# Kernel optimization log

Measured on AMD Instinct MI355X. Metric: run time of the kernel, lower is better.

Reference implementation:

```python
import jax, jax.numpy as jnp
import numpy as np

N, E, DIN, GB, GD, LB, LD, G = 50000, 640000, 64, 128, 4, 256, 2, 1024


def setup_inputs() -> dict:
    key = jax.random.key(0)
    ks = jax.random.split(key, 20)
    p = lambda k, shape: (jax.random.normal(k, shape, dtype=jnp.float32) * 0.05)
    return {
        "x": jax.random.normal(ks[0], (N, DIN), dtype=jnp.float32),
        "edge_index": jax.random.randint(ks[1], (2, E), 0, N, dtype=jnp.int64),
        "batch": jnp.sort(jax.random.randint(ks[2], (N,), 0, G, dtype=jnp.int64)),
        "num_graphs": G,
        "W0": p(ks[3], (DIN, GB)), "b0": p(ks[4], (GB,)),
        "Wg": p(ks[5], (GD, GB, GB)), "bg": p(ks[6], (GD, GB)),
        "gamma_g": jnp.ones((GD, GB), jnp.float32), "beta_g": jnp.zeros((GD, GB), jnp.float32),
        "Wl0": p(ks[7], (GB, LB)), "bl0": p(ks[8], (LB,)),
        "Wl": p(ks[9], (LD, LB, LB)), "bl": p(ks[10], (LD, LB)),
        "gamma_l": jnp.ones((LD, LB), jnp.float32), "beta_l": jnp.zeros((LD, LB), jnp.float32),
        "Wout": p(ks[11], (LB, 2)), "bout": p(ks[12], (2,)),
    }


def reference(x, edge_index, batch, num_graphs, W0, b0, Wg, bg, gamma_g, beta_g,
              Wl0, bl0, Wl, bl, gamma_l, beta_l, Wout, bout):
    n = x.shape[0]
    src, dst = edge_index[0], edge_index[1]
    # GCN degree normalization with self loops: deg = 1 + in-degree
    deg = jax.ops.segment_sum(jnp.ones(src.shape[0], x.dtype), dst, num_segments=n) + 1.0
    dinv = jax.lax.rsqrt(deg)                 # deg^{-1/2}
    enorm = dinv[src] * dinv[dst]             # [E] edge norm
    snorm = dinv * dinv                       # [N] self-loop norm (deg^{-1})

    def gcn(h, W, b):
        hw = h @ W                                            # [N, GB]
        agg = jax.ops.segment_sum(hw[src] * enorm[:, None], dst, num_segments=n)
        return agg + hw * snorm[:, None] + b

    def bn(h, g, bt):  # training-mode batchnorm (biased var), eps=1e-5
        m = h.mean(0)
        v = h.var(0)
        return (h - m) * jax.lax.rsqrt(v + 1e-5) * g + bt

    h = jax.nn.relu(gcn(x, W0, b0))
    for i in range(Wg.shape[0]):
        h = jax.nn.relu(bn(gcn(h, Wg[i], bg[i]), gamma_g[i], beta_g[i]))
    # global_add_pool
    hp = jax.ops.segment_sum(h, batch, num_segments=num_graphs)  # [G, GB]
    h = jax.nn.relu(hp @ Wl0 + bl0)
    for i in range(Wl.shape[0]):
        h = jax.nn.relu(bn(h @ Wl[i] + bl[i], gamma_l[i], beta_l[i]))
    return h @ Wout + bout
```

## Files before the change

kernel.cpp:

```cpp
#include <hip/hip_runtime.h>

#define NN 50000
#define EE 640000
#define DINv 64
#define GBv 128
#define GDv 4
#define LBv 256
#define LDv 2
#define GGv 1024

#define NB 196
#define BCAP 4096
#define BTILE 4096
#define NBT ((EE + BTILE - 1) / BTILE)

#define NTILES ((NN + 63) / 64)
#define UPN (NN * 16)
#define CONVN (DINv * GBv + GDv * GBv * GBv)
#define ZEXT 320

typedef _Float16 f16x8 __attribute__((ext_vector_type(8)));
typedef float f32x4 __attribute__((ext_vector_type(4)));

__device__ __forceinline__ float h2f(ushort u) {
  union { ushort u; _Float16 h; } x;
  x.u = u;
  return (float)x.h;
}
__device__ __forceinline__ ushort f2h(float f) {
  union { ushort u; _Float16 h; } x;
  x.h = (_Float16)f;
  return x.u;
}


__global__ __launch_bounds__(256) void k_bucket(const int* __restrict__ ei,
                                                int* __restrict__ bcnt,
                                                uint* __restrict__ bkt) {
  __shared__ int lcnt[NB];
  __shared__ int lbase[NB];
  __shared__ int gbase[NB];
  __shared__ int ls[256];
  __shared__ uint stage[BTILE];
  __shared__ ushort sb[BTILE];
  int tid = threadIdx.x;
  int t0 = blockIdx.x * BTILE;
  int cnt = min(BTILE, EE - t0);
  for (int i = tid; i < NB; i += 256) lcnt[i] = 0;
  __syncthreads();

  uint en[16];
  int bb[16], rk[16];
  int nper = (cnt + 255) >> 8;
  for (int k = 0; k < nper; k++) {
    int e = k * 256 + tid;
    if (e < cnt) {
      int src = ei[t0 + e];
      int dst = ei[EE + t0 + e];
      int b = dst >> 8;
      en[k] = ((uint)src << 8) | (uint)(dst & 255);
      bb[k] = b;
      rk[k] = atomicAdd(&lcnt[b], 1);
    } else {
      bb[k] = -1;
    }
  }
  __syncthreads();

  int v = (tid < NB) ? lcnt[tid] : 0;
  ls[tid] = v;
  __syncthreads();
  for (int off = 1; off < 256; off <<= 1) {
    int t = (tid >= off) ? ls[tid - off] : 0;
    __syncthreads();
    ls[tid] += t;
    __syncthreads();
  }
  if (tid < NB) {
    lbase[tid] = ls[tid] - v;
    gbase[tid] = atomicAdd(&bcnt[tid], v);
  }
  __syncthreads();

  for (int k = 0; k < nper; k++) {
    if (bb[k] >= 0) {
      int slot = lbase[bb[k]] + rk[k];
      stage[slot] = en[k];
      sb[slot] = (ushort)bb[k];
    }
  }
  __syncthreads();

  for (int i = tid; i < cnt; i += 256) {
    int b = sb[i];
    bkt[(size_t)b * BCAP + gbase[b] + (i - lbase[b])] = stage[i];
  }
}


__global__ __launch_bounds__(256) void k_csr(const uint* __restrict__ bkt,
                                             const int* __restrict__ bcnt,
                                             int* __restrict__ offs,
                                             float* __restrict__ dinv,
                                             int* __restrict__ col,
                                             int* __restrict__ deg,
                                             int* __restrict__ ghist) {
  __shared__ int lhist[256];
  __shared__ int lofs[256];
  __shared__ int lcur[256];
  __shared__ int lsb[256];
  __shared__ int lh2[64];
  int b = blockIdx.x;
  int tid = threadIdx.x;
  int bv = (tid < NB) ? bcnt[tid] : 0;
  lsb[tid] = bv;
  lhist[tid] = 0;
  if (tid < 64) lh2[tid] = 0;
  __syncthreads();
  for (int off = 1; off < 256; off <<= 1) {
    int t = (tid >= off) ? lsb[tid - off] : 0;
    __syncthreads();
    lsb[tid] += t;
    __syncthreads();
  }
  int cnt = bcnt[b];
  int rawbase = lsb[b] - cnt;
  int pbase = ((rawbase + 7) & ~7) + b * 4096;
  const uint* B = bkt + (size_t)b * BCAP;
  for (int i = tid; i < cnt; i += 256) atomicAdd(&lhist[B[i] & 255], 1);
  __syncthreads();
  int v = lhist[tid];
  int pv = (v + 15) & ~15;
  lofs[tid] = pv;
  __syncthreads();
  for (int off = 1; off < 256; off <<= 1) {
    int t = (tid >= off) ? lofs[tid - off] : 0;
    __syncthreads();
    lofs[tid] += t;
    __syncthreads();
  }
  int excl = lofs[tid] - pv;
  int n = b * 256 + tid;
  if (n < NN) {
    offs[n] = pbase + excl;
    dinv[n] = rsqrtf((float)(v + 1));
    deg[n] = v;
    atomicAdd(&lh2[min(v, 63)], 1);
    for (int k = v; k < pv; k++) col[pbase + excl + k] = NN;
  }
  lcur[tid] = excl;
  __syncthreads();
  if (tid < 64 && lh2[tid]) atomicAdd(&ghist[tid], lh2[tid]);
  if (b == 0 && tid == 0) dinv[NN] = 0.f;
  for (int i = tid; i < cnt; i += 256) {
    uint e = B[i];
    int p = atomicAdd(&lcur[e & 255], 1);
    col[pbase + p] = (int)(e >> 8);
  }
}


__global__ __launch_bounds__(256) void k_dperm(const int* __restrict__ deg,
                                               const int* __restrict__ ghist,
                                               int* __restrict__ gcur,
                                               int* __restrict__ perm) {
  __shared__ int lhist[64];
  __shared__ int lbase[64];
  int tid = threadIdx.x;
  if (tid < 64) lhist[tid] = 0;
  __syncthreads();
  int n = blockIdx.x * 256 + tid;
  int d = 0, rk = 0;
  if (n < NN) {
    d = min(deg[n], 63);
    rk = atomicAdd(&lhist[d], 1);
  }
  __syncthreads();
  if (tid < 64) {
    int s = 0;
    for (int i = tid + 1; i < 64; i++) s += ghist[i];
    if (lhist[tid]) lbase[tid] = s + atomicAdd(&gcur[tid], lhist[tid]);
  }
  __syncthreads();
  if (n < NN) perm[lbase[d] + rk] = n;
}


__global__ __launch_bounds__(256) void k_prep(const float* __restrict__ x,
                                              const float* __restrict__ dinv,
                                              const float* __restrict__ W0,
                                              const float* __restrict__ Wg,
                                              ushort* __restrict__ u,
                                              ushort* __restrict__ Wt0,
                                              ushort* __restrict__ Wtg,
                                              ushort* __restrict__ g1,
                                              ushort* __restrict__ g3) {
  int idx = blockIdx.x * 256 + threadIdx.x;
  if (idx < UPN) {
    int n = idx >> 4;
    float4 v = ((const float4*)x)[idx];
    float d = dinv[n];
    union { ushort us[4]; uint2 q; } o;
    o.us[0] = f2h(v.x * d);
    o.us[1] = f2h(v.y * d);
    o.us[2] = f2h(v.z * d);
    o.us[3] = f2h(v.w * d);
    ((uint2*)u)[idx] = o.q;
  } else {
    int j = idx - UPN;
    if (j < DINv * GBv) {
      int c = j >> 6, k = j & 63;
      Wt0[j] = f2h(W0[k * GBv + c]);
    } else if (j < CONVN) {
      int e = j - DINv * GBv;
      int i = e >> 14, rem = e & 16383;
      int c = rem >> 7, k = rem & 127;
      Wtg[e] = f2h(Wg[i * GBv * GBv + k * GBv + c]);
    } else if (j < CONVN + ZEXT) {
      int z = j - CONVN;
      if (z < 64) u[(size_t)NN * DINv + z] = 0;
      else if (z < 192) g1[(size_t)NN * GBv + (z - 64)] = 0;
      else g3[(size_t)NN * GBv + (z - 192)] = 0;
    }
  }
}


__global__ __launch_bounds__(256) void k_bn(const ushort* __restrict__ G,
                                            const float* __restrict__ st,
                                            const float* __restrict__ gamma,
                                            const float* __restrict__ beta,
                                            const float* __restrict__ dinv,
                                            ushort* __restrict__ Gt) {
  __shared__ float sS[128], sT[128];
  int tid = threadIdx.x;
  if (tid < 128) {
    float mu = st[tid] * (1.f / NN);
    float var = st[128 + tid] * (1.f / NN) - mu * mu;
    float s = rsqrtf(var + 1e-5f) * gamma[tid];
    sS[tid] = s;
    sT[tid] = beta[tid] - mu * s;
  }
  __syncthreads();
  int idx = blockIdx.x * 256 + tid;
  if (idx < NN * 16) {
    int n = idx >> 4, c0 = (idx & 15) * 8;
    float dv = dinv[n];
    union { uint4 v4; ushort us[8]; } in, o;
    in.v4 = ((const uint4*)G)[idx];
#pragma unroll
    for (int v = 0; v < 8; v++)
      o.us[v] = f2h(fmaxf(h2f(in.us[v]) * sS[c0 + v] + sT[c0 + v], 0.f) * dv);
    ((uint4*)Gt)[idx] = o.v4;
  }
}


template <int K, bool STATS, bool OUTF>
__global__ __launch_bounds__(512, 2) void k_layer(const ushort* __restrict__ Gin,
                                                  const int* __restrict__ col,
                                                  const int* __restrict__ offs,
                                                  const int* __restrict__ deg,
                                                  const float* __restrict__ dinv,
                                                  const int* __restrict__ perm,
                                                  const ushort* __restrict__ Wt,
                                                  const float* __restrict__ bias,
                                                  float* __restrict__ stG,
                                                  ushort* __restrict__ Gout) {
  constexpr int VEC = K / 16;
  constexpr int KP = K + 8;
  constexpr int CP = 136;
  constexpr bool REUSE = (K == 128);
  __shared__ __attribute__((aligned(16))) _Float16 sW[128 * KP];
  __shared__ __attribute__((aligned(16))) _Float16 sA[64 * KP];
  __shared__ float sB[128];
  __shared__ float ssum[128], ssq[128];
  __shared__ float sDn[64];
  _Float16* sC = REUSE ? sA : sW;
  int tid = threadIdx.x;

  {
    constexpr int CH = K / 8;
    for (int i = tid; i < 128 * CH; i += 512) {
      int c = i / CH, ch = i - c * CH;
      *(uint4*)&sW[c * KP + ch * 8] = ((const uint4*)Wt)[i];
    }
  }
  if (tid < 128) {
    sB[tid] = bias[tid];
    if constexpr (STATS) {
      ssum[tid] = 0.f;
      ssq[tid] = 0.f;
    }
  }

  int w = tid >> 6, lane = tid & 63;
  int quad = lane >> 4, m = lane & 15;
  int row0 = blockIdx.x * 64;

  union U { uint4 v4; uint2 v2; ushort us[8]; };
  auto loadrow = [&](int s) {
    U u;
    const ushort* p = Gin + (long)s * K + m * VEC;
    if constexpr (VEC == 8) u.v4 = *(const uint4*)p;
    else u.v2 = *(const uint2*)p;
    return u;
  };

  for (int rnd = 0; rnd < 2; rnd++) {
    int r = rnd * 32 + w * 4 + quad;
    int idx = row0 + r;
    float acc[VEC];
#pragma unroll
    for (int v = 0; v < VEC; v++) acc[v] = 0.f;
    float dn = 0.f;
    if (idx < NN) {
      int n = perm[idx];
      dn = dinv[n];
      auto addrow = [&](U u) {
#pragma unroll
        for (int v = 0; v < VEC; v++) acc[v] += h2f(u.us[v]);
      };

      int s0 = offs[n];
      int pcnt = (deg[n] + 15) & ~15;
      const int* cp = col + s0;

      U uself = loadrow(n);
      U uu[16];
      if (pcnt > 0) {
        int4 c0 = *(const int4*)(cp + 0);
        int4 c1 = *(const int4*)(cp + 4);
        int4 c2 = *(const int4*)(cp + 8);
        int4 c3 = *(const int4*)(cp + 12);
        uu[0] = loadrow(c0.x);
        uu[1] = loadrow(c0.y);
        uu[2] = loadrow(c0.z);
        uu[3] = loadrow(c0.w);
        uu[4] = loadrow(c1.x);
        uu[5] = loadrow(c1.y);
        uu[6] = loadrow(c1.z);
        uu[7] = loadrow(c1.w);
        uu[8] = loadrow(c2.x);
        uu[9] = loadrow(c2.y);
        uu[10] = loadrow(c2.z);
        uu[11] = loadrow(c2.w);
        uu[12] = loadrow(c3.x);
        uu[13] = loadrow(c3.y);
        uu[14] = loadrow(c3.z);
        uu[15] = loadrow(c3.w);
      }
      addrow(uself);
      for (int j = 0; j < pcnt; j += 16) {
        bool more = (j + 16) < pcnt;
        int4 n0, n1, n2, n3;
        if (more) {
          n0 = *(const int4*)(cp + j + 16);
          n1 = *(const int4*)(cp + j + 20);
          n2 = *(const int4*)(cp + j + 24);
          n3 = *(const int4*)(cp + j + 28);
        }
#pragma unroll
        for (int t = 0; t < 16; t++) addrow(uu[t]);
        if (more) {
          uu[0] = loadrow(n0.x);
          uu[1] = loadrow(n0.y);
          uu[2] = loadrow(n0.z);
          uu[3] = loadrow(n0.w);
          uu[4] = loadrow(n1.x);
          uu[5] = loadrow(n1.y);
          uu[6] = loadrow(n1.z);
          uu[7] = loadrow(n1.w);
          uu[8] = loadrow(n2.x);
          uu[9] = loadrow(n2.y);
          uu[10] = loadrow(n2.z);
          uu[11] = loadrow(n2.w);
          uu[12] = loadrow(n3.x);
          uu[13] = loadrow(n3.y);
          uu[14] = loadrow(n3.z);
          uu[15] = loadrow(n3.w);
        }
      }
    }
    if constexpr (OUTF) {
      if (m == 0) sDn[r] = dn;
    }
    U o;
#pragma unroll
    for (int v = 0; v < VEC; v++) o.us[v] = f2h(acc[v] * dn);
    _Float16* ap = &sA[r * KP + m * VEC];
    if constexpr (VEC == 8) *(uint4*)ap = o.v4;
    else *(uint2*)ap = o.v2;
  }
  __syncthreads();

  int wr = w >> 1, wc = w & 1;
  f32x4 acc2[4];
#pragma unroll
  for (int ct = 0; ct < 4; ct++) acc2[ct] = (f32x4){0.f, 0.f, 0.f, 0.f};
  const _Float16* pa = &sA[(16 * wr + m) * KP + quad * 8];
#pragma unroll
  for (int ks = 0; ks < K; ks += 32) {
    f16x8 a = *(const f16x8*)(pa + ks);
#pragma unroll
    for (int ct = 0; ct < 4; ct++) {
      int c = wc * 64 + ct * 16 + m;
      f16x8 bfr = *(const f16x8*)&sW[c * KP + ks + quad * 8];
      acc2[ct] = __builtin_amdgcn_mfma_f32_16x16x32_f16(a, bfr, acc2[ct], 0, 0, 0);
    }
  }

  int crow = 16 * wr + quad * 4;
  float ps[4], pq[4];
  if constexpr (STATS) {
#pragma unroll
    for (int ct = 0; ct < 4; ct++) {
      int c = wc * 64 + ct * 16 + m;
      float bb = sB[c];
      ps[ct] = 0.f;
      pq[ct] = 0.f;
#pragma unroll
      for (int r = 0; r < 4; r++) {
        if (row0 + crow + r < NN) {
          float g = acc2[ct][r] + bb;
          ps[ct] += g;
          pq[ct] += g * g;
        }
      }
    }
  }
  __syncthreads();

  float dvr[4];
  if constexpr (OUTF) {
#pragma unroll
    for (int r = 0; r < 4; r++) dvr[r] = sDn[crow + r];
  }
#pragma unroll
  for (int ct = 0; ct < 4; ct++) {
    int c = wc * 64 + ct * 16 + m;
    float bb = sB[c];
#pragma unroll
    for (int r = 0; r < 4; r++) {
      float y = acc2[ct][r] + bb;
      if constexpr (OUTF) y = fmaxf(y, 0.f) * dvr[r];
      sC[(crow + r) * CP + c] = (_Float16)y;
    }
  }
  __syncthreads();

  {
    int r = tid >> 3;
    int c0 = (tid & 7) * 16;
    int idx2 = row0 + r;
    if (idx2 < NN) {
      int node = perm[idx2];
      const uint4* srcp = (const uint4*)&sC[r * CP + c0];
      uint4* dst = (uint4*)(Gout + (long)node * 128 + c0);
      dst[0] = srcp[0];
      dst[1] = srcp[1];
    }
  }

  if constexpr (STATS) {
#pragma unroll
    for (int ct = 0; ct < 4; ct++) {
      float s = ps[ct], q = pq[ct];
      s += __shfl_xor(s, 16);
      q += __shfl_xor(q, 16);
      s += __shfl_xor(s, 32);
      q += __shfl_xor(q, 32);
      if (quad == 0) {
        atomicAdd(&ssum[wc * 64 + ct * 16 + m], s);
        atomicAdd(&ssq[wc * 64 + ct * 16 + m], q);
      }
    }
    __syncthreads();
    if (tid < 128) {
      int c = (tid + blockIdx.x * 8) & 127;
      atomicAdd(&stG[c], ssum[c]);
      atomicAdd(&stG[128 + c], ssq[c]);
    }
  }
}


__global__ __launch_bounds__(128) void k_pool2(const ushort* __restrict__ G,
                                               const float* __restrict__ st,
                                               const float* __restrict__ gamma,
                                               const float* __restrict__ beta,
                                               const int* __restrict__ batch,
                                               float* __restrict__ hp) {
  __shared__ int sse[2];
  int g = blockIdx.x;
  int c = threadIdx.x;
  if (c < 2) {
    int key = g + c;
    int lo = 0, hi = NN;
    while (lo < hi) {
      int mid = (lo + hi) >> 1;
      if (batch[mid] < key) lo = mid + 1;
      else hi = mid;
    }
    sse[c] = lo;
  }
  __syncthreads();
  int s = sse[0], e = sse[1];
  float m = st[c] * (1.f / NN);
  float v = st[128 + c] * (1.f / NN) - m * m;
  float sc = rsqrtf(v + 1e-5f) * gamma[c];
  float tc = beta[c] - m * sc;
  float a0 = 0.f, a1 = 0.f, a2 = 0.f, a3 = 0.f;
  int n = s;
  for (; n + 3 < e; n += 4) {
    float g0 = h2f(G[(long)(n + 0) * 128 + c]);
    float g1 = h2f(G[(long)(n + 1) * 128 + c]);
    float g2 = h2f(G[(long)(n + 2) * 128 + c]);
    float g3 = h2f(G[(long)(n + 3) * 128 + c]);
    a0 += fmaxf(g0 * sc + tc, 0.f);
    a1 += fmaxf(g1 * sc + tc, 0.f);
    a2 += fmaxf(g2 * sc + tc, 0.f);
    a3 += fmaxf(g3 * sc + tc, 0.f);
  }
  for (; n < e; n++) a0 += fmaxf(h2f(G[(long)n * 128 + c]) * sc + tc, 0.f);
  hp[(long)g * 128 + c] = (a0 + a1) + (a2 + a3);
}


__global__ void k_colstats(const float* __restrict__ X, int rows, float* __restrict__ st) {
  int c = threadIdx.x;
  int C = blockDim.x;
  float s = 0.f, q = 0.f;
  for (int r = blockIdx.x; r < rows; r += gridDim.x) {
    float v = X[(long)r * C + c];
    s += v;
    q += v * v;
  }
  atomicAdd(&st[c], s);
  atomicAdd(&st[C + c], q);
}


template <int KIN, int MODE>
__global__ __launch_bounds__(256) void k_fc(const float* __restrict__ X,
                                            const float* __restrict__ W,
                                            const float* __restrict__ b,
                                            const float* __restrict__ st,
                                            const float* __restrict__ gamma,
                                            const float* __restrict__ beta,
                                            float* __restrict__ Y) {
  __shared__ float sx[KIN];
  int g = blockIdx.x;
  int c = threadIdx.x;
  for (int k = c; k < KIN; k += 256) {
    float v = X[(long)g * KIN + k];
    if constexpr (MODE == 2) {
      float m = st[k] * (1.f / GGv);
      float var = st[KIN + k] * (1.f / GGv) - m * m;
      v = fmaxf((v - m) * rsqrtf(var + 1e-5f) * gamma[k] + beta[k], 0.f);
    }
    sx[k] = v;
  }
  __syncthreads();
  float acc = b[c];
#pragma unroll 8
  for (int k = 0; k < KIN; k++) acc += sx[k] * W[(long)k * 256 + c];
  Y[(long)g * 256 + c] = (MODE == 0) ? fmaxf(acc, 0.f) : acc;
}

__global__ __launch_bounds__(256) void k_out(const float* __restrict__ X,
                                             const float* __restrict__ st,
                                             const float* __restrict__ gamma,
                                             const float* __restrict__ beta,
                                             const float* __restrict__ Wout,
                                             const float* __restrict__ bout,
                                             float* __restrict__ out) {
  int g = blockIdx.x * 4 + (threadIdx.x >> 6);
  int l = threadIdx.x & 63;
  float a0 = 0.f, a1 = 0.f;
  for (int k = l; k < LBv; k += 64) {
    float z = X[(long)g * LBv + k];
    float m = st[k] * (1.f / GGv);
    float var = st[LBv + k] * (1.f / GGv) - m * m;
    float x = fmaxf((z - m) * rsqrtf(var + 1e-5f) * gamma[k] + beta[k], 0.f);
    a0 += x * Wout[2 * k];
    a1 += x * Wout[2 * k + 1];
  }
  for (int off = 32; off > 0; off >>= 1) {
    a0 += __shfl_down(a0, off);
    a1 += __shfl_down(a1, off);
  }
  if (l == 0) {
    out[2 * g] = a0 + bout[0];
    out[2 * g + 1] = a1 + bout[1];
  }
}


extern "C" void kernel_launch(void* const* d_in, const int* in_sizes, int n_in,
                              void* d_out, int out_size, void* d_ws, size_t ws_size,
                              hipStream_t stream) {
  const float* x = (const float*)d_in[0];
  const int* ei = (const int*)d_in[1];
  const int* batch = (const int*)d_in[2];
  const float* W0 = (const float*)d_in[4];
  const float* b0 = (const float*)d_in[5];
  const float* Wg = (const float*)d_in[6];
  const float* bg = (const float*)d_in[7];
  const float* gamma_g = (const float*)d_in[8];
  const float* beta_g = (const float*)d_in[9];
  const float* Wl0 = (const float*)d_in[10];
  const float* bl0 = (const float*)d_in[11];
  const float* Wl = (const float*)d_in[12];
  const float* bl = (const float*)d_in[13];
  const float* gamma_l = (const float*)d_in[14];
  const float* beta_l = (const float*)d_in[15];
  const float* Wout = (const float*)d_in[16];
  const float* bout = (const float*)d_in[17];
  float* out = (float*)d_out;

  char* w = (char*)d_ws;
  auto alloc = [&](size_t bytes) {
    void* p = (void*)w;
    w += (bytes + 255) & ~(size_t)255;
    return p;
  };
  int* bcnt = (int*)alloc((size_t)NB * 4);
  float* stAll = (float*)alloc((size_t)(4 * 256 + 2 * 512) * 4);
  int* ghist = (int*)alloc((size_t)64 * 4);
  int* gcur = (int*)alloc((size_t)64 * 4);
  size_t zspan = (char*)w - (char*)bcnt;
  uint* bkt = (uint*)alloc((size_t)NB * BCAP * 4);
  int* offs = (int*)alloc((size_t)(NN + 1) * 4);
  int* col = (int*)alloc((size_t)(EE + NB * 4096 + 8192) * 4);
  float* dinv = (float*)alloc((size_t)(NN + 1) * 4);
  int* deg = (int*)alloc((size_t)NN * 4);
  int* perm = (int*)alloc((size_t)NN * 4);
  ushort* u = (ushort*)alloc((size_t)(NN + 1) * DINv * 2);
  ushort* g1 = (ushort*)alloc((size_t)(NN + 1) * GBv * 2);
  ushort* g2 = (ushort*)alloc((size_t)(NN + 1) * GBv * 2);
  ushort* g3 = (ushort*)alloc((size_t)(NN + 1) * GBv * 2);
  ushort* Wt0 = (ushort*)alloc((size_t)DINv * GBv * 2);
  ushort* Wtg = (ushort*)alloc((size_t)GDv * GBv * GBv * 2);
  float* hp = (float*)alloc((size_t)GGv * GBv * 4);
  float* m1 = (float*)alloc((size_t)GGv * LBv * 4);
  float* m2 = (float*)alloc((size_t)GGv * LBv * 4);

  float* stg = stAll;
  float* sth0 = stAll + 4 * 256;
  float* sth1 = sth0 + 512;

  hipMemsetAsync(bcnt, 0, zspan, stream);

  k_bucket<<<NBT, 256, 0, stream>>>(ei, bcnt, bkt);
  k_csr<<<NB, 256, 0, stream>>>(bkt, bcnt, offs, dinv, col, deg, ghist);
  k_dperm<<<NB, 256, 0, stream>>>(deg, ghist, gcur, perm);
  k_prep<<<(UPN + CONVN + ZEXT + 255) / 256, 256, 0, stream>>>(x, dinv, W0, Wg, u, Wt0,
                                                               Wtg, g1, g3);

  const int BNG = (NN * 16 + 255) / 256;

  k_layer<64, false, true><<<NTILES, 512, 0, stream>>>(u, col, offs, deg, dinv, perm,
                                                       Wt0, b0, nullptr, g1);
  k_layer<128, true, false><<<NTILES, 512, 0, stream>>>(g1, col, offs, deg, dinv, perm,
                                                        Wtg, bg, stg, g2);
  for (int i = 1; i < GDv; i++) {
    k_bn<<<BNG, 256, 0, stream>>>(g2, stg + (size_t)(i - 1) * 256,
                                  gamma_g + (size_t)(i - 1) * GBv,
                                  beta_g + (size_t)(i - 1) * GBv, dinv, g3);
    k_layer<128, true, false><<<NTILES, 512, 0, stream>>>(
        g3, col, offs, deg, dinv, perm, Wtg + (size_t)i * GBv * GBv,
        bg + (size_t)i * GBv, stg + (size_t)i * 256, g2);
  }

  k_pool2<<<GGv, 128, 0, stream>>>(g2, stg + 3 * 256, gamma_g + 3 * GBv, beta_g + 3 * GBv,
                                   batch, hp);

  k_fc<GBv, 0><<<GGv, 256, 0, stream>>>(hp, Wl0, bl0, nullptr, nullptr, nullptr, m1);
  k_fc<LBv, 1><<<GGv, 256, 0, stream>>>(m1, Wl, bl, nullptr, nullptr, nullptr, m2);
  k_colstats<<<256, LBv, 0, stream>>>(m2, GGv, sth0);
  k_fc<LBv, 2><<<GGv, 256, 0, stream>>>(m2, Wl + (size_t)LBv * LBv, bl + LBv, sth0,
                                        gamma_l, beta_l, m1);
  k_colstats<<<256, LBv, 0, stream>>>(m1, GGv, sth1);
  k_out<<<GGv / 4, 256, 0, stream>>>(m1, sth1, gamma_l + LBv, beta_l + LBv, Wout, bout, out);
}
```

Baseline: 470.2 us.

## Shrink gather batch, drop shared weight staging, raise k_layer occupancy

Neighbor lists are now padded to multiples of 8 instead of 16, and the gather loop prefetches 8 rows per step, which cuts wasted padded loads and the register footprint. The weight matrix is no longer copied into shared memory; MFMA B-fragments are read directly from global memory, so the kernel needs much less LDS. Launch bounds are raised from 2 to 8 blocks per SM to allow more resident waves. In exchange, weight reads now depend on cache hits, and the tighter register budget may cause spills or expose gather latency more.

Result: slower. 694.8 us (+47.8%).

```diff
diff --git a/kernel.cpp b/kernel.cpp
--- a/kernel.cpp
+++ b/kernel.cpp
@@ -130,7 +130,7 @@
   for (int i = tid; i < cnt; i += 256) atomicAdd(&lhist[B[i] & 255], 1);
   __syncthreads();
   int v = lhist[tid];
-  int pv = (v + 15) & ~15;
+  int pv = (v + 7) & ~7;
   lofs[tid] = pv;
   __syncthreads();
   for (int off = 1; off < 256; off <<= 1) {
@@ -257,7 +257,7 @@
 
 
 template <int K, bool STATS, bool OUTF>
-__global__ __launch_bounds__(512, 2) void k_layer(const ushort* __restrict__ Gin,
+__global__ __launch_bounds__(512, 8) void k_layer(const ushort* __restrict__ Gin,
                                                   const int* __restrict__ col,
                                                   const int* __restrict__ offs,
                                                   const int* __restrict__ deg,
@@ -270,22 +270,13 @@
   constexpr int VEC = K / 16;
   constexpr int KP = K + 8;
   constexpr int CP = 136;
-  constexpr bool REUSE = (K == 128);
-  __shared__ __attribute__((aligned(16))) _Float16 sW[128 * KP];
-  __shared__ __attribute__((aligned(16))) _Float16 sA[64 * KP];
+  __shared__ __attribute__((aligned(16))) _Float16 sA[64 * 136];
   __shared__ float sB[128];
   __shared__ float ssum[128], ssq[128];
   __shared__ float sDn[64];
-  _Float16* sC = REUSE ? sA : sW;
+  _Float16* sC = sA;
   int tid = threadIdx.x;
 
-  {
-    constexpr int CH = K / 8;
-    for (int i = tid; i < 128 * CH; i += 512) {
-      int c = i / CH, ch = i - c * CH;
-      *(uint4*)&sW[c * KP + ch * 8] = ((const uint4*)Wt)[i];
-    }
-  }
   if (tid < 128) {
     sB[tid] = bias[tid];
     if constexpr (STATS) {
@@ -323,16 +314,14 @@
       };
 
       int s0 = offs[n];
-      int pcnt = (deg[n] + 15) & ~15;
+      int pcnt = (deg[n] + 7) & ~7;
       const int* cp = col + s0;
 
       U uself = loadrow(n);
-      U uu[16];
+      U uu[8];
       if (pcnt > 0) {
         int4 c0 = *(const int4*)(cp + 0);
         int4 c1 = *(const int4*)(cp + 4);
-        int4 c2 = *(const int4*)(cp + 8);
-        int4 c3 = *(const int4*)(cp + 12);
         uu[0] = loadrow(c0.x);
         uu[1] = loadrow(c0.y);
         uu[2] = loadrow(c0.z);
@@ -341,27 +330,17 @@
         uu[5] = loadrow(c1.y);
         uu[6] = loadrow(c1.z);
         uu[7] = loadrow(c1.w);
-        uu[8] = loadrow(c2.x);
-        uu[9] = loadrow(c2.y);
-        uu[10] = loadrow(c2.z);
-        uu[11] = loadrow(c2.w);
-        uu[12] = loadrow(c3.x);
-        uu[13] = loadrow(c3.y);
-        uu[14] = loadrow(c3.z);
-        uu[15] = loadrow(c3.w);
       }
       addrow(uself);
-      for (int j = 0; j < pcnt; j += 16) {
-        bool more = (j + 16) < pcnt;
-        int4 n0, n1, n2, n3;
+      for (int j = 0; j < pcnt; j += 8) {
+        bool more = (j + 8) < pcnt;
+        int4 n0, n1;
         if (more) {
-          n0 = *(const int4*)(cp + j + 16);
-          n1 = *(const int4*)(cp + j + 20);
-          n2 = *(const int4*)(cp + j + 24);
-          n3 = *(const int4*)(cp + j + 28);
+          n0 = *(const int4*)(cp + j + 8);
+          n1 = *(const int4*)(cp + j + 12);
         }
 #pragma unroll
-        for (int t = 0; t < 16; t++) addrow(uu[t]);
+        for (int t = 0; t < 8; t++) addrow(uu[t]);
         if (more) {
           uu[0] = loadrow(n0.x);
           uu[1] = loadrow(n0.y);
@@ -371,14 +350,6 @@
           uu[5] = loadrow(n1.y);
           uu[6] = loadrow(n1.z);
           uu[7] = loadrow(n1.w);
-          uu[8] = loadrow(n2.x);
-          uu[9] = loadrow(n2.y);
-          uu[10] = loadrow(n2.z);
-          uu[11] = loadrow(n2.w);
-          uu[12] = loadrow(n3.x);
-          uu[13] = loadrow(n3.y);
-          uu[14] = loadrow(n3.z);
-          uu[15] = loadrow(n3.w);
         }
       }
     }
@@ -405,7 +376,7 @@
 #pragma unroll
     for (int ct = 0; ct < 4; ct++) {
       int c = wc * 64 + ct * 16 + m;
-      f16x8 bfr = *(const f16x8*)&sW[c * KP + ks + quad * 8];
+      f16x8 bfr = *(const f16x8*)((const _Float16*)Wt + (size_t)c * K + ks + quad * 8);
       acc2[ct] = __builtin_amdgcn_mfma_f32_16x16x32_f16(a, bfr, acc2[ct], 0, 0, 0);
     }
   }
```
